# Optimization experiments

Hardware: AMD Instinct MI355X
Metric: run time of the kernel (lower is better)

The kernel has to match this reference:

```python
import jax, jax.numpy as jnp
import numpy as np

B, P, IN, H, OUT, K = 8192, 64, 3, 20, 10, 4

_elu = jax.nn.elu

def _knn(x, valid):
    # x: [B,P,H], valid: [B,P] bool -> k nearest valid neighbors (excluding self)
    sq = jnp.sum(x * x, -1)
    score = 2.0 * jnp.einsum('bpd,bqd->bpq', x, x) - sq[:, :, None] - sq[:, None, :]  # -||xi-xj||^2
    Pn = x.shape[1]
    score = jnp.where(jnp.eye(Pn, dtype=bool)[None], -jnp.inf, score)
    score = jnp.where(valid[:, None, :], score, -jnp.inf)
    return jax.lax.top_k(score, K)[1]  # [B,P,K]

def _gather(x, idx):
    b, p, k = idx.shape
    return jnp.take_along_axis(x, idx.reshape(b, p * k)[..., None], axis=1).reshape(b, p, k, x.shape[-1])

def _edgeconv(x, idx, valid, W1, b1, W2, b2):
    # EdgeConv message MLP([x_i, x_j - x_i]) with aggr='add'
    xi = x[:, :, None, :]
    xj = _gather(x, idx)
    feat = jnp.concatenate([jnp.broadcast_to(xi, xj.shape), xj - xi], axis=-1)  # [B,P,K,2H]
    m = _elu(feat @ W1 + b1)
    m = _elu(m @ W2 + b2)
    vj = jnp.take_along_axis(valid, idx.reshape(idx.shape[0], -1), axis=1).reshape(idx.shape)
    h = jnp.sum(m * vj[..., None].astype(m.dtype), axis=2)
    return h * valid[..., None].astype(h.dtype)

def _pool(h, idx, valid):
    # graclus-style coarsening: merge each node with its nearest neighbor, max-pool features
    Pn = h.shape[1]
    nn0 = idx[..., 0]
    cluster = jnp.minimum(jnp.arange(Pn)[None, :], nn0)
    c = jnp.where(valid, cluster, Pn)  # invalid nodes -> dummy slot Pn
    def one(hh, cc, vv):
        neg = jnp.where(vv[:, None], hh, -jnp.inf)
        pooled = jnp.full((Pn + 1, hh.shape[-1]), -jnp.inf, hh.dtype).at[cc].max(neg)[:Pn]
        cnt = jnp.zeros(Pn + 1, hh.dtype).at[cc].add(vv.astype(hh.dtype))[:Pn]
        nv = cnt > 0
        return jnp.where(nv[:, None], pooled, 0.0), nv
    return jax.vmap(one)(h, c, valid)

def setup_inputs():
    key = jax.random.key(0)
    ks = jax.random.split(key, 12)
    g = lambda k, s: 0.2 * jax.random.normal(k, s, jnp.float32)
    z = lambda n: jnp.zeros((n,), jnp.float32)
    inp = {'x': jax.random.normal(ks[0], (B, P, IN), jnp.float32)}
    inp['Wi0'] = g(ks[1], (IN, H)); inp['bi0'] = z(H)
    inp['Wi1'] = g(ks[2], (H, H)); inp['bi1'] = z(H)
    inp['Wi2'] = g(ks[3], (H, H)); inp['bi2'] = z(H)
    inp['We0a'] = g(ks[4], (2 * H, H)); inp['be0a'] = z(H)
    inp['We0b'] = g(ks[5], (H, H)); inp['be0b'] = z(H)
    inp['We1a'] = g(ks[6], (2 * H, H)); inp['be1a'] = z(H)
    inp['We1b'] = g(ks[7], (H, H)); inp['be1b'] = z(H)
    inp['Wo0'] = g(ks[8], (H, H)); inp['bo0'] = z(H)
    inp['Wo1'] = g(ks[9], (H, H)); inp['bo1'] = z(H)
    inp['Wo2'] = g(ks[10], (H, OUT)); inp['bo2'] = z(OUT)
    return inp

def reference(x, Wi0, bi0, Wi1, bi1, Wi2, bi2, We0a, be0a, We0b, be0b, We1a, be1a, We1b, be1b, Wo0, bo0, Wo1, bo1, Wo2, bo2):
    valid = jnp.ones(x.shape[:2], bool)
    # input network (in_layers=3)
    h = _elu(x @ Wi0 + bi0)
    h = _elu(h @ Wi1 + bi1)
    h = _elu(h @ Wi2 + bi2)
    # agg_layers=2: dynamic kNN + EdgeConv(add) + hierarchical coarsening
    for Wa, ba, Wb, bb in ((We0a, be0a, We0b, be0b), (We1a, be1a, We1b, be1b)):
        idx = _knn(h, valid)
        h = _edgeconv(h, idx, valid, Wa, ba, Wb, bb)
        h, valid = _pool(h, idx, valid)
    # global max pool over surviving clusters
    g = jnp.max(jnp.where(valid[..., None], h, -jnp.inf), axis=1)
    # output network (out_layers=3)
    o = _elu(g @ Wo0 + bo0)
    o = _elu(o @ Wo1 + bo1)
    logits = o @ Wo2 + bo2
    return jax.nn.log_softmax(logits, axis=1)
```

## Files before the change

### kernel.cpp

```cpp
#include <hip/hip_runtime.h>
#include <math.h>

#define HH 20
#define HP 21
#define PP 64

#define W_WI0 0
#define W_BI0 60
#define W_WI1 80
#define W_BI1 480
#define W_WI2 500
#define W_BI2 900
#define W_EB0 920
#define W_EB1 2160
#define W_TOT 3400

__device__ __forceinline__ double expm1_neg(double v) {
    if (v <= -40.0) return -1.0;
    const double LOG2E  = 1.4426950408889634074e+00;
    const double LN2_HI = 6.93147180369123816490e-01;
    const double LN2_LO = 1.90821492927058770002e-10;
    double nd = rint(v * LOG2E);
    double r  = fma(-nd, LN2_HI, v);
    r = fma(-nd, LN2_LO, r);
    double p = 2.75573192239858925110e-06;
    p = fma(p, r, 2.48015873015873015873e-05);
    p = fma(p, r, 1.98412698412698412698e-04);
    p = fma(p, r, 1.38888888888888888889e-03);
    p = fma(p, r, 8.33333333333333333333e-03);
    p = fma(p, r, 4.16666666666666666667e-02);
    p = fma(p, r, 1.66666666666666666667e-01);
    p = fma(p, r, 5.0e-01);
    p = fma(p, r, 1.0);
    p = fma(p, r, 1.0);
    long long n = (long long)nd;
    double sc = __builtin_bit_cast(double, (unsigned long long)(1023ll + n) << 52);
    return fma(p, sc, -1.0);
}
__device__ __forceinline__ double elu_d(double v) { return v > 0.0 ? v : expm1_neg(v); }
__device__ __forceinline__ float  elu_f(float v)  { return v > 0.0f ? v : expm1f(v); }

__device__ __forceinline__ unsigned long long fenc64(double f) {
    unsigned long long u = __builtin_bit_cast(unsigned long long, f);
    return (u & 0x8000000000000000ull) ? ~u : (u | 0x8000000000000000ull);
}
__device__ __forceinline__ double fdec64(unsigned long long u) {
    unsigned long long b = (u & 0x8000000000000000ull) ? (u & 0x7fffffffffffffffull) : ~u;
    return __builtin_bit_cast(double, b);
}

__global__ __launch_bounds__(256) void prep_weights(
    const float* __restrict__ Wi0, const float* __restrict__ bi0,
    const float* __restrict__ Wi1, const float* __restrict__ bi1,
    const float* __restrict__ Wi2, const float* __restrict__ bi2,
    const float* __restrict__ We0a, const float* __restrict__ be0a,
    const float* __restrict__ We0b, const float* __restrict__ be0b,
    const float* __restrict__ We1a, const float* __restrict__ be1a,
    const float* __restrict__ We1b, const float* __restrict__ be1b,
    double* __restrict__ ws)
{
    const int t = threadIdx.x;
    #define CV(off, src, n) for (int i = t; i < (n); i += 256) ws[(off) + i] = (double)(src)[i];
    CV(W_WI0, Wi0, 60)  CV(W_BI0, bi0, 20)
    CV(W_WI1, Wi1, 400) CV(W_BI1, bi1, 20)
    CV(W_WI2, Wi2, 400) CV(W_BI2, bi2, 20)
    for (int i = t; i < 400; i += 256) {
        ws[W_EB0 +       i] = (double)We0a[i] - (double)We0a[400 + i];
        ws[W_EB0 + 400 + i] = (double)We0a[400 + i];
        ws[W_EB0 + 800 + i] = (double)We0b[i];
        ws[W_EB1 +       i] = (double)We1a[i] - (double)We1a[400 + i];
        ws[W_EB1 + 400 + i] = (double)We1a[400 + i];
        ws[W_EB1 + 800 + i] = (double)We1b[i];
    }
    for (int i = t; i < 20; i += 256) {
        ws[W_EB0 + 1200 + i] = (double)be0a[i];
        ws[W_EB0 + 1220 + i] = (double)be0b[i];
        ws[W_EB1 + 1200 + i] = (double)be1a[i];
        ws[W_EB1 + 1220 + i] = (double)be1b[i];
    }
    #undef CV
}

#define SBAR() __builtin_amdgcn_sched_barrier(0)

__global__ __launch_bounds__(64, 1) void dgcnn_fused(
    const float* __restrict__ x,
    const double* __restrict__ wd,
    const float* __restrict__ Wo0, const float* __restrict__ bo0,
    const float* __restrict__ Wo1, const float* __restrict__ bo1,
    const float* __restrict__ Wo2, const float* __restrict__ bo2,
    float* __restrict__ out)
{
    const int b = blockIdx.x;
    const int p = threadIdx.x;

    __shared__ __align__(16) double hbuf[PP][HP];
    __shared__ __align__(16) double wlds[1280];
    __shared__ int ivld[PP];
    __shared__ int cflag[PP];

    double h[HH];
    {
        const size_t xb = (size_t)b * (PP * 3) + (size_t)p * 3;
        const double x0 = (double)x[xb + 0];
        const double x1 = (double)x[xb + 1];
        const double x2 = (double)x[xb + 2];
        double t[HH];
        #pragma unroll
        for (int j = 0; j < HH; ++j)
            t[j] = fma(x2, wd[W_WI0 + 2*HH + j],
                   fma(x1, wd[W_WI0 + HH + j],
                   fma(x0, wd[W_WI0 + j], wd[W_BI0 + j])));
        #pragma unroll
        for (int j5 = 0; j5 < HH; j5 += 5) {
            #pragma unroll
            for (int j = j5; j < j5 + 5; ++j) t[j] = elu_d(t[j]);
            SBAR();
        }
        #pragma unroll
        for (int j = 0; j < HH; ++j) h[j] = wd[W_BI1 + j];
        #pragma unroll 2
        for (int d = 0; d < HH; ++d) {
            const double td = t[d];
            #pragma unroll
            for (int j = 0; j < HH; ++j)
                h[j] = fma(td, wd[W_WI1 + d*HH + j], h[j]);
        }
        #pragma unroll
        for (int j5 = 0; j5 < HH; j5 += 5) {
            #pragma unroll
            for (int j = j5; j < j5 + 5; ++j) t[j] = elu_d(h[j]);
            SBAR();
        }
        #pragma unroll
        for (int j = 0; j < HH; ++j) h[j] = wd[W_BI2 + j];
        #pragma unroll 2
        for (int d = 0; d < HH; ++d) {
            const double td = t[d];
            #pragma unroll
            for (int j = 0; j < HH; ++j)
                h[j] = fma(td, wd[W_WI2 + d*HH + j], h[j]);
        }
        #pragma unroll
        for (int j5 = 0; j5 < HH; j5 += 5) {
            #pragma unroll
            for (int j = j5; j < j5 + 5; ++j) h[j] = elu_d(h[j]);
            SBAR();
        }
    }
    int myvalid = 1;

    #pragma unroll 1
    for (int blk = 0; blk < 2; ++blk) {
        const double* bundle = wd + (blk ? W_EB1 : W_EB0);
        #pragma unroll
        for (int i = 0; i < 20; ++i) {
            const int idx = i * 64 + p;
            wlds[idx] = (idx < 1240) ? bundle[idx] : 0.0;
        }

        double sqp = 0.0;
        #pragma unroll
        for (int d = 0; d < HH; ++d) sqp = fma(h[d], h[d], sqp);
        #pragma unroll
        for (int j = 0; j < HH; ++j) hbuf[p][j] = h[j];
        hbuf[p][HH] = sqp;
        ivld[p] = myvalid;
        __syncthreads();

        unsigned long long e0 = 0ull, e1 = 0ull, e2 = 0ull, e3 = 0ull;
        #pragma unroll 2
        for (int q = 0; q < PP; ++q) {
            double dot = 0.0;
            #pragma unroll
            for (int d = 0; d < HH; ++d)
                dot = fma(hbuf[q][d], h[d], dot);
            double s = 2.0*dot - sqp - hbuf[q][HH];
            if (q == p || ivld[q] == 0) s = -INFINITY;
            const unsigned long long e =
                (fenc64(s) & ~63ull) | (unsigned long long)(63 - q);
            const bool b0 = e > e0;
            const bool b1 = e > e1;
            const bool b2 = e > e2;
            const bool b3 = e > e3;
            e3 = b2 ? e2 : (b3 ? e : e3);
            e2 = b1 ? e1 : (b2 ? e : e2);
            e1 = b0 ? e0 : (b1 ? e : e1);
            e0 = b0 ? e  : e0;
        }
        SBAR();
        const int i0 = 63 - (int)(e0 & 63ull);

        double base[HH];
        #pragma unroll
        for (int j = 0; j < HH; ++j) base[j] = wlds[1200 + j];
        #pragma unroll 2
        for (int d = 0; d < HH; ++d) {
            const double hd = h[d];
            #pragma unroll
            for (int j = 0; j < HH; ++j)
                base[j] = fma(hd, wlds[d*HH + j], base[j]);
        }
        double y[HH];
        #pragma unroll
        for (int j = 0; j < HH; ++j) y[j] = 0.0;
        #pragma unroll 2
        for (int d = 0; d < HH; ++d) {
            const double hd = h[d];
            #pragma unroll
            for (int j = 0; j < HH; ++j)
                y[j] = fma(hd, wlds[400 + d*HH + j], y[j]);
        }
        __syncthreads();
        #pragma unroll
        for (int j = 0; j < HH; ++j) hbuf[p][j] = y[j];
        __syncthreads();

        double hsum[HH];
        #pragma unroll
        for (int j = 0; j < HH; ++j) hsum[j] = 0.0;

        #pragma unroll 1
        for (int k = 0; k < 4; ++k) {
            const unsigned long long ek = (k == 0) ? e0 : (k == 1) ? e1 : (k == 2) ? e2 : e3;
            const int jn = 63 - (int)(ek & 63ull);
            const double vn = (double)ivld[jn];

            double m1[HH];
            #pragma unroll
            for (int j = 0; j < HH; ++j) m1[j] = base[j] + hbuf[jn][j];
            #pragma unroll
            for (int j5 = 0; j5 < HH; j5 += 5) {
                #pragma unroll
                for (int j = j5; j < j5 + 5; ++j) m1[j] = elu_d(m1[j]);
                SBAR();
            }

            #pragma unroll
            for (int j5 = 0; j5 < HH; j5 += 5) {
                #pragma unroll
                for (int j = j5; j < j5 + 5; ++j) {
                    double a0 = wlds[1220 + j];
                    #pragma unroll
                    for (int d = 0; d < HH; ++d)
                        a0 = fma(m1[d], wlds[800 + d*HH + j], a0);
                    hsum[j] = fma(elu_d(a0), vn, hsum[j]);
                }
                SBAR();
            }
        }
        {
            const double vpd = (double)myvalid;
            #pragma unroll
            for (int j = 0; j < HH; ++j) hsum[j] *= vpd;
        }
        __syncthreads();

        unsigned long long* pbuf = (unsigned long long*)&hbuf[0][0];
        #pragma unroll
        for (int j = 0; j < HH; ++j) pbuf[p*HP + j] = 0ull;
        cflag[p] = 0;
        __syncthreads();
        {
            const int c = min(p, i0);
            if (myvalid) {
                cflag[c] = 1;
                #pragma unroll
                for (int j = 0; j < HH; ++j)
                    atomicMax(&pbuf[c*HP + j], fenc64(hsum[j]));
            }
        }
        __syncthreads();
        {
            const int nv = cflag[p];
            myvalid = nv;
            #pragma unroll
            for (int j = 0; j < HH; ++j)
                h[j] = nv ? fdec64(pbuf[p*HP + j]) : 0.0;
        }
        __syncthreads();
    }

    float hf[HH];
    #pragma unroll
    for (int j = 0; j < HH; ++j) hf[j] = myvalid ? (float)h[j] : -INFINITY;
    #pragma unroll
    for (int s = 1; s < 64; s <<= 1) {
        #pragma unroll
        for (int j = 0; j < HH; ++j)
            hf[j] = fmaxf(hf[j], __shfl_xor(hf[j], s));
    }

    float o1[HH], o2[HH], lg[10];
    #pragma unroll
    for (int j = 0; j < HH; ++j) o1[j] = bo0[j];
    #pragma unroll 2
    for (int d = 0; d < HH; ++d) {
        #pragma unroll
        for (int j = 0; j < HH; ++j) o1[j] = fmaf(hf[d], Wo0[d*HH + j], o1[j]);
    }
    #pragma unroll
    for (int j = 0; j < HH; ++j) o1[j] = elu_f(o1[j]);
    #pragma unroll
    for (int j = 0; j < HH; ++j) o2[j] = bo1[j];
    #pragma unroll 2
    for (int d = 0; d < HH; ++d) {
        #pragma unroll
        for (int j = 0; j < HH; ++j) o2[j] = fmaf(o1[d], Wo1[d*HH + j], o2[j]);
    }
    #pragma unroll
    for (int j = 0; j < HH; ++j) o2[j] = elu_f(o2[j]);
    #pragma unroll
    for (int j = 0; j < 10; ++j) lg[j] = bo2[j];
    #pragma unroll 2
    for (int d = 0; d < HH; ++d) {
        #pragma unroll
        for (int j = 0; j < 10; ++j) lg[j] = fmaf(o2[d], Wo2[d*10 + j], lg[j]);
    }
    float m = lg[0];
    #pragma unroll
    for (int j = 1; j < 10; ++j) m = fmaxf(m, lg[j]);
    float ssum = 0.0f;
    #pragma unroll
    for (int j = 0; j < 10; ++j) ssum += expf(lg[j] - m);
    const float lse = m + logf(ssum);
    if (p < 10) {
        float v = 0.0f;
        #pragma unroll
        for (int j = 0; j < 10; ++j) v = (p == j) ? lg[j] : v;
        out[(size_t)b * 10 + p] = v - lse;
    }
}

extern "C" void kernel_launch(void* const* d_in, const int* in_sizes, int n_in,
                              void* d_out, int out_size, void* d_ws, size_t ws_size,
                              hipStream_t stream) {
    const float* x    = (const float*)d_in[0];
    const float* Wi0  = (const float*)d_in[1];
    const float* bi0  = (const float*)d_in[2];
    const float* Wi1  = (const float*)d_in[3];
    const float* bi1  = (const float*)d_in[4];
    const float* Wi2  = (const float*)d_in[5];
    const float* bi2  = (const float*)d_in[6];
    const float* We0a = (const float*)d_in[7];
    const float* be0a = (const float*)d_in[8];
    const float* We0b = (const float*)d_in[9];
    const float* be0b = (const float*)d_in[10];
    const float* We1a = (const float*)d_in[11];
    const float* be1a = (const float*)d_in[12];
    const float* We1b = (const float*)d_in[13];
    const float* be1b = (const float*)d_in[14];
    const float* Wo0  = (const float*)d_in[15];
    const float* bo0  = (const float*)d_in[16];
    const float* Wo1  = (const float*)d_in[17];
    const float* bo1  = (const float*)d_in[18];
    const float* Wo2  = (const float*)d_in[19];
    const float* bo2  = (const float*)d_in[20];
    float* out = (float*)d_out;
    double* ws = (double*)d_ws;

    prep_weights<<<dim3(1), dim3(256), 0, stream>>>(
        Wi0, bi0, Wi1, bi1, Wi2, bi2,
        We0a, be0a, We0b, be0b, We1a, be1a, We1b, be1b, ws);

    dgcnn_fused<<<dim3(8192), dim3(64), 0, stream>>>(
        x, ws, Wo0, bo0, Wo1, bo1, Wo2, bo2, out);
}
```

Before: 849.7 us.

## Unroll EdgeConv blocks, run second block in fp32 with fast ELU

Splits the two-iteration EdgeConv loop into two specialized blocks. The first block stays in fp64 but drops validity checks, since all nodes are valid there, reads weights directly from global memory instead of staging them in LDS, and uses a vectorized double2 kNN dot product with four independent accumulators. The second block runs the message MLP, ELU (via __expf) and max-pool atomics in fp32 with a dedicated fp32 weight copy, while keeping fp64 for the kNN scores. This is meant to cut fp64 ALU cost and LDS traffic, at the risk of numerical differences in the second block.

```diff
diff --git a/kernel.cpp b/kernel.cpp
--- a/kernel.cpp
+++ b/kernel.cpp
@@ -2,7 +2,8 @@
 #include <math.h>
 
 #define HH 20
-#define HP 21
+#define HS 22
+#define HSF 21
 #define PP 64
 
 #define W_WI0 0
@@ -12,8 +13,7 @@
 #define W_WI2 500
 #define W_BI2 900
 #define W_EB0 920
-#define W_EB1 2160
-#define W_TOT 3400
+#define W_F1  2160
 
 __device__ __forceinline__ double expm1_neg(double v) {
     if (v <= -40.0) return -1.0;
@@ -39,6 +39,7 @@
 }
 __device__ __forceinline__ double elu_d(double v) { return v > 0.0 ? v : expm1_neg(v); }
 __device__ __forceinline__ float  elu_f(float v)  { return v > 0.0f ? v : expm1f(v); }
+__device__ __forceinline__ float  elu_fast(float v) { return v > 0.0f ? v : __expf(v) - 1.0f; }
 
 __device__ __forceinline__ unsigned long long fenc64(double f) {
     unsigned long long u = __builtin_bit_cast(unsigned long long, f);
@@ -47,6 +48,14 @@
 __device__ __forceinline__ double fdec64(unsigned long long u) {
     unsigned long long b = (u & 0x8000000000000000ull) ? (u & 0x7fffffffffffffffull) : ~u;
     return __builtin_bit_cast(double, b);
+}
+__device__ __forceinline__ unsigned fenc32(float f) {
+    unsigned u = __float_as_uint(f);
+    return (u & 0x80000000u) ? ~u : (u | 0x80000000u);
+}
+__device__ __forceinline__ float fdec32(unsigned u) {
+    unsigned b = (u & 0x80000000u) ? (u & 0x7fffffffu) : ~u;
+    return __uint_as_float(b);
 }
 
 __global__ __launch_bounds__(256) void prep_weights(
@@ -60,6 +69,7 @@
     double* __restrict__ ws)
 {
     const int t = threadIdx.x;
+    float* wf = (float*)(ws + W_F1);
     #define CV(off, src, n) for (int i = t; i < (n); i += 256) ws[(off) + i] = (double)(src)[i];
     CV(W_WI0, Wi0, 60)  CV(W_BI0, bi0, 20)
     CV(W_WI1, Wi1, 400) CV(W_BI1, bi1, 20)
@@ -68,15 +78,15 @@
         ws[W_EB0 +       i] = (double)We0a[i] - (double)We0a[400 + i];
         ws[W_EB0 + 400 + i] = (double)We0a[400 + i];
         ws[W_EB0 + 800 + i] = (double)We0b[i];
-        ws[W_EB1 +       i] = (double)We1a[i] - (double)We1a[400 + i];
-        ws[W_EB1 + 400 + i] = (double)We1a[400 + i];
-        ws[W_EB1 + 800 + i] = (double)We1b[i];
+        wf[      i] = We1a[i] - We1a[400 + i];
+        wf[400 + i] = We1a[400 + i];
+        wf[800 + i] = We1b[i];
     }
     for (int i = t; i < 20; i += 256) {
         ws[W_EB0 + 1200 + i] = (double)be0a[i];
         ws[W_EB0 + 1220 + i] = (double)be0b[i];
-        ws[W_EB1 + 1200 + i] = (double)be1a[i];
-        ws[W_EB1 + 1220 + i] = (double)be1b[i];
+        wf[1200 + i] = be1a[i];
+        wf[1220 + i] = be1b[i];
     }
     #undef CV
 }
@@ -94,10 +104,11 @@
     const int b = blockIdx.x;
     const int p = threadIdx.x;
 
-    __shared__ __align__(16) double hbuf[PP][HP];
-    __shared__ __align__(16) double wlds[1280];
+    __shared__ __align__(16) double hbuf[PP][HS];
     __shared__ int ivld[PP];
     __shared__ int cflag[PP];
+
+    const float* wf = (const float*)(wd + W_F1);
 
     double h[HH];
     {
@@ -148,17 +159,131 @@
             SBAR();
         }
     }
-    int myvalid = 1;
-
-    #pragma unroll 1
-    for (int blk = 0; blk < 2; ++blk) {
-        const double* bundle = wd + (blk ? W_EB1 : W_EB0);
-        #pragma unroll
-        for (int i = 0; i < 20; ++i) {
-            const int idx = i * 64 + p;
-            wlds[idx] = (idx < 1240) ? bundle[idx] : 0.0;
-        }
-
+
+    int myvalid;
+    int i0_b0;
+    {
+        double sqp = 0.0;
+        #pragma unroll
+        for (int d = 0; d < HH; ++d) sqp = fma(h[d], h[d], sqp);
+        #pragma unroll
+        for (int j = 0; j < HH; ++j) hbuf[p][j] = h[j];
+        hbuf[p][HH] = sqp;
+        __syncthreads();
+
+        unsigned long long e0 = 0ull, e1 = 0ull, e2 = 0ull, e3 = 0ull;
+        #pragma unroll 2
+        for (int q = 0; q < PP; ++q) {
+            const double2* rowq = (const double2*)&hbuf[q][0];
+            double a0 = 0.0, a1 = 0.0, a2 = 0.0, a3 = 0.0;
+            #pragma unroll
+            for (int t2 = 0; t2 < 10; t2 += 2) {
+                const double2 r0 = rowq[t2];
+                const double2 r1 = rowq[t2 + 1];
+                a0 = fma(r0.x, h[2*t2],     a0);
+                a1 = fma(r0.y, h[2*t2 + 1], a1);
+                a2 = fma(r1.x, h[2*t2 + 2], a2);
+                a3 = fma(r1.y, h[2*t2 + 3], a3);
+            }
+            double s = 2.0*((a0 + a1) + (a2 + a3)) - sqp - hbuf[q][HH];
+            if (q == p) s = -INFINITY;
+            const unsigned long long e =
+                (fenc64(s) & ~63ull) | (unsigned long long)(63 - q);
+            const bool b0 = e > e0;
+            const bool b1 = e > e1;
+            const bool b2 = e > e2;
+            const bool b3 = e > e3;
+            e3 = b2 ? e2 : (b3 ? e : e3);
+            e2 = b1 ? e1 : (b2 ? e : e2);
+            e1 = b0 ? e0 : (b1 ? e : e1);
+            e0 = b0 ? e  : e0;
+        }
+        SBAR();
+        i0_b0 = 63 - (int)(e0 & 63ull);
+
+        double base[HH], y[HH];
+        #pragma unroll
+        for (int j = 0; j < HH; ++j) base[j] = wd[W_EB0 + 1200 + j];
+        #pragma unroll 2
+        for (int d = 0; d < HH; ++d) {
+            const double hd = h[d];
+            #pragma unroll
+            for (int j = 0; j < HH; ++j)
+                base[j] = fma(hd, wd[W_EB0 + d*HH + j], base[j]);
+        }
+        #pragma unroll
+        for (int j = 0; j < HH; ++j) y[j] = 0.0;
+        #pragma unroll 2
+        for (int d = 0; d < HH; ++d) {
+            const double hd = h[d];
+            #pragma unroll
+            for (int j = 0; j < HH; ++j)
+                y[j] = fma(hd, wd[W_EB0 + 400 + d*HH + j], y[j]);
+        }
+        __syncthreads();
+        #pragma unroll
+        for (int j = 0; j < HH; ++j) hbuf[p][j] = y[j];
+        __syncthreads();
+
+        double hsum[HH];
+        #pragma unroll
+        for (int j = 0; j < HH; ++j) hsum[j] = 0.0;
+
+        #pragma unroll 1
+        for (int k = 0; k < 4; ++k) {
+            const unsigned long long ek = (k == 0) ? e0 : (k == 1) ? e1 : (k == 2) ? e2 : e3;
+            const int jn = 63 - (int)(ek & 63ull);
+
+            double m1[HH];
+            #pragma unroll
+            for (int j = 0; j < HH; ++j) m1[j] = base[j] + hbuf[jn][j];
+            #pragma unroll
+            for (int j5 = 0; j5 < HH; j5 += 5) {
+                #pragma unroll
+                for (int j = j5; j < j5 + 5; ++j) m1[j] = elu_d(m1[j]);
+                SBAR();
+            }
+            #pragma unroll
+            for (int j5 = 0; j5 < HH; j5 += 5) {
+                #pragma unroll
+                for (int j = j5; j < j5 + 5; ++j) {
+                    double a0 = wd[W_EB0 + 1220 + j];
+                    #pragma unroll
+                    for (int d = 0; d < HH; ++d)
+                        a0 = fma(m1[d], wd[W_EB0 + 800 + d*HH + j], a0);
+                    hsum[j] += elu_d(a0);
+                }
+                SBAR();
+            }
+        }
+        __syncthreads();
+
+        unsigned long long* pbuf = (unsigned long long*)&hbuf[0][0];
+        #pragma unroll
+        for (int j = 0; j < HH; ++j) pbuf[p*HS + j] = 0ull;
+        cflag[p] = 0;
+        __syncthreads();
+        {
+            const int c = min(p, i0_b0);
+            cflag[c] = 1;
+            #pragma unroll
+            for (int j = 0; j < HH; ++j)
+                atomicMax(&pbuf[c*HS + j], fenc64(hsum[j]));
+        }
+        __syncthreads();
+        {
+            const int nv = cflag[p];
+            myvalid = nv;
+            #pragma unroll
+            for (int j = 0; j < HH; ++j)
+                h[j] = nv ? fdec64(pbuf[p*HS + j]) : 0.0;
+        }
+        __syncthreads();
+    }
+
+    float hpool[HH];
+    int   vfinal;
+    {
         double sqp = 0.0;
         #pragma unroll
         for (int d = 0; d < HH; ++d) sqp = fma(h[d], h[d], sqp);
@@ -171,11 +296,18 @@
         unsigned long long e0 = 0ull, e1 = 0ull, e2 = 0ull, e3 = 0ull;
         #pragma unroll 2
         for (int q = 0; q < PP; ++q) {
-            double dot = 0.0;
-            #pragma unroll
-            for (int d = 0; d < HH; ++d)
-                dot = fma(hbuf[q][d], h[d], dot);
-            double s = 2.0*dot - sqp - hbuf[q][HH];
+            const double2* rowq = (const double2*)&hbuf[q][0];
+            double a0 = 0.0, a1 = 0.0, a2 = 0.0, a3 = 0.0;
+            #pragma unroll
+            for (int t2 = 0; t2 < 10; t2 += 2) {
+                const double2 r0 = rowq[t2];
+                const double2 r1 = rowq[t2 + 1];
+                a0 = fma(r0.x, h[2*t2],     a0);
+                a1 = fma(r0.y, h[2*t2 + 1], a1);
+                a2 = fma(r1.x, h[2*t2 + 2], a2);
+                a3 = fma(r1.y, h[2*t2 + 3], a3);
+            }
+            double s = 2.0*((a0 + a1) + (a2 + a3)) - sqp - hbuf[q][HH];
             if (q == p || ivld[q] == 0) s = -INFINITY;
             const unsigned long long e =
                 (fenc64(s) & ~63ull) | (unsigned long long)(63 - q);
@@ -191,74 +323,67 @@
         SBAR();
         const int i0 = 63 - (int)(e0 & 63ull);
 
-        double base[HH];
-        #pragma unroll
-        for (int j = 0; j < HH; ++j) base[j] = wlds[1200 + j];
-        #pragma unroll 2
-        for (int d = 0; d < HH; ++d) {
-            const double hd = h[d];
-            #pragma unroll
-            for (int j = 0; j < HH; ++j)
-                base[j] = fma(hd, wlds[d*HH + j], base[j]);
-        }
-        double y[HH];
-        #pragma unroll
-        for (int j = 0; j < HH; ++j) y[j] = 0.0;
-        #pragma unroll 2
-        for (int d = 0; d < HH; ++d) {
-            const double hd = h[d];
-            #pragma unroll
-            for (int j = 0; j < HH; ++j)
-                y[j] = fma(hd, wlds[400 + d*HH + j], y[j]);
-        }
-        __syncthreads();
-        #pragma unroll
-        for (int j = 0; j < HH; ++j) hbuf[p][j] = y[j];
-        __syncthreads();
-
-        double hsum[HH];
-        #pragma unroll
-        for (int j = 0; j < HH; ++j) hsum[j] = 0.0;
+        float hf[HH];
+        #pragma unroll
+        for (int j = 0; j < HH; ++j) hf[j] = (float)h[j];
+
+        float basef[HH], yf[HH];
+        #pragma unroll
+        for (int j = 0; j < HH; ++j) basef[j] = wf[1200 + j];
+        #pragma unroll 2
+        for (int d = 0; d < HH; ++d) {
+            const float hd = hf[d];
+            #pragma unroll
+            for (int j = 0; j < HH; ++j)
+                basef[j] = fmaf(hd, wf[d*HH + j], basef[j]);
+        }
+        #pragma unroll
+        for (int j = 0; j < HH; ++j) yf[j] = 0.0f;
+        #pragma unroll 2
+        for (int d = 0; d < HH; ++d) {
+            const float hd = hf[d];
+            #pragma unroll
+            for (int j = 0; j < HH; ++j)
+                yf[j] = fmaf(hd, wf[400 + d*HH + j], yf[j]);
+        }
+        __syncthreads();
+        float* ybuf = (float*)&hbuf[0][0];
+        #pragma unroll
+        for (int j = 0; j < HH; ++j) ybuf[p*HSF + j] = yf[j];
+        __syncthreads();
+
+        float hsumf[HH];
+        #pragma unroll
+        for (int j = 0; j < HH; ++j) hsumf[j] = 0.0f;
 
         #pragma unroll 1
         for (int k = 0; k < 4; ++k) {
             const unsigned long long ek = (k == 0) ? e0 : (k == 1) ? e1 : (k == 2) ? e2 : e3;
             const int jn = 63 - (int)(ek & 63ull);
-            const double vn = (double)ivld[jn];
-
-            double m1[HH];
-            #pragma unroll
-            for (int j = 0; j < HH; ++j) m1[j] = base[j] + hbuf[jn][j];
-            #pragma unroll
-            for (int j5 = 0; j5 < HH; j5 += 5) {
+            const float vn = (float)ivld[jn];
+
+            float m1f[HH];
+            #pragma unroll
+            for (int j = 0; j < HH; ++j) m1f[j] = elu_fast(basef[j] + ybuf[jn*HSF + j]);
+            #pragma unroll
+            for (int j = 0; j < HH; ++j) {
+                float a0 = wf[1220 + j];
                 #pragma unroll
-                for (int j = j5; j < j5 + 5; ++j) m1[j] = elu_d(m1[j]);
-                SBAR();
-            }
-
-            #pragma unroll
-            for (int j5 = 0; j5 < HH; j5 += 5) {
-                #pragma unroll
-                for (int j = j5; j < j5 + 5; ++j) {
-                    double a0 = wlds[1220 + j];
-                    #pragma unroll
-                    for (int d = 0; d < HH; ++d)
-                        a0 = fma(m1[d], wlds[800 + d*HH + j], a0);
-                    hsum[j] = fma(elu_d(a0), vn, hsum[j]);
-                }
-                SBAR();
+                for (int d = 0; d < HH; ++d)
+                    a0 = fmaf(m1f[d], wf[800 + d*HH + j], a0);
+                hsumf[j] = fmaf(elu_fast(a0), vn, hsumf[j]);
             }
         }
         {
-            const double vpd = (double)myvalid;
-            #pragma unroll
-            for (int j = 0; j < HH; ++j) hsum[j] *= vpd;
-        }
-        __syncthreads();
-
-        unsigned long long* pbuf = (unsigned long long*)&hbuf[0][0];
-        #pragma unroll
-        for (int j = 0; j < HH; ++j) pbuf[p*HP + j] = 0ull;
+            const float vp = (float)myvalid;
+            #pragma unroll
+            for (int j = 0; j < HH; ++j) hsumf[j] *= vp;
+        }
+        __syncthreads();
+
+        unsigned* pb32 = (unsigned*)&hbuf[0][0];
+        #pragma unroll
+        for (int j = 0; j < HH; ++j) pb32[p*HSF + j] = 0u;
         cflag[p] = 0;
         __syncthreads();
         {
@@ -267,23 +392,21 @@
                 cflag[c] = 1;
                 #pragma unroll
                 for (int j = 0; j < HH; ++j)
-                    atomicMax(&pbuf[c*HP + j], fenc64(hsum[j]));
+                    atomicMax(&pb32[c*HSF + j], fenc32(hsumf[j]));
             }
         }
         __syncthreads();
         {
-            const int nv = cflag[p];
-            myvalid = nv;
-            #pragma unroll
-            for (int j = 0; j < HH; ++j)
-                h[j] = nv ? fdec64(pbuf[p*HP + j]) : 0.0;
-        }
-        __syncthreads();
+            vfinal = cflag[p];
+            #pragma unroll
+            for (int j = 0; j < HH; ++j)
+                hpool[j] = vfinal ? fdec32(pb32[p*HSF + j]) : 0.0f;
+        }
     }
 
     float hf[HH];
     #pragma unroll
-    for (int j = 0; j < HH; ++j) hf[j] = myvalid ? (float)h[j] : -INFINITY;
+    for (int j = 0; j < HH; ++j) hf[j] = vfinal ? hpool[j] : -INFINITY;
     #pragma unroll
     for (int s = 1; s < 64; s <<= 1) {
         #pragma unroll
```

Measured after the change: 1.049 ms. 23.5% more time.
